# Optimization experiments

Measured on AMD Instinct MI355X. Metric: run time of the kernel, lower is better.

Reference implementation:

```python
import jax, jax.numpy as jnp
import numpy as np

BS, T, N, DIM = 16, 2048, 2048, 128

def setup_inputs() -> dict:
    key = jax.random.key(0)
    k1, k2, k3 = jax.random.split(key, 3)
    aud_feats = jax.random.normal(k1, (BS, T, DIM), dtype=jnp.float32)
    semantic_feats = jax.random.normal(k2, (BS, N, DIM), dtype=jnp.float32)
    W = jax.random.normal(k3, (1, 3 * DIM), dtype=jnp.float32) * 0.02
    b = jnp.zeros((1,), dtype=jnp.float32)
    return {"aud_feats": aud_feats, "semantic_feats": semantic_feats, "W": W, "b": b}


def reference(aud_feats, semantic_feats, W, b):
    # S[b,i,j] = Linear(cat(h_t, h_n, h_t*h_n)) decomposed into three rank-1 pieces
    dim = aud_feats.shape[-1]
    w1 = W[0, :dim]
    w2 = W[0, dim:2 * dim]
    w3 = W[0, 2 * dim:]
    S = (jnp.einsum('btd,d->bt', aud_feats, w1)[:, :, None]
         + jnp.einsum('bnd,d->bn', semantic_feats, w2)[:, None, :]
         + jnp.einsum('btd,bnd->btn', aud_feats * w3, semantic_feats)
         + b[0])  # [bs, t, n]
    at = jax.nn.softmax(S, axis=2)                     # attend over semantic tokens
    bw = jax.nn.softmax(jnp.max(S, axis=2), axis=1)    # [bs, t]
    h_con_a2 = jnp.einsum('bt,btd->bd', bw, aud_feats)[:, None, :]   # [bs,1,d], broadcasts
    h_con_w = jnp.einsum('btn,bnd->btd', at, semantic_feats)          # [bs,t,d]
    flow_matrix = jnp.concatenate(
        [aud_feats, h_con_w, aud_feats * h_con_w, aud_feats * h_con_a2], axis=2)
    return flow_matrix
```

## Files before the change

kernel.cpp:

```cpp
#include <hip/hip_runtime.h>
#include <stdint.h>

#define BSZ 16
#define TT  2048
#define NSEM 2048
#define DIM 128
#define ORS 1024
#define PSTR 68

typedef __attribute__((ext_vector_type(8))) short short8;
typedef __attribute__((ext_vector_type(4))) float floatx4;

__device__ __forceinline__ unsigned short f2bf(float f){
  unsigned u = __float_as_uint(f);
  return (unsigned short)((u + 0x7fffu + ((u >> 16) & 1u)) >> 16);
}
__device__ __forceinline__ void ld8f(const float* p, float* v){
  floatx4 a = *(const floatx4*)p;
  floatx4 b = *(const floatx4*)(p + 4);
  v[0]=a[0]; v[1]=a[1]; v[2]=a[2]; v[3]=a[3];
  v[4]=b[0]; v[5]=b[1]; v[6]=b[2]; v[7]=b[3];
}
__device__ __forceinline__ void gload_lds16(const unsigned short* g, unsigned short* l){
  __builtin_amdgcn_global_load_lds((const __attribute__((address_space(1))) void*)g,
                                   (__attribute__((address_space(3))) void*)l, 16, 0, 0);
}


__global__ __launch_bounds__(256) void prep_kernel(const float* __restrict__ sem,
                                                   const float* __restrict__ W,
                                                   float* __restrict__ colB,
                                                   unsigned short* __restrict__ outw){
  __shared__ unsigned short tile[DIM * 72];
  const int tid = threadIdx.x;
  const int b  = blockIdx.x >> 5;
  const int n0 = (blockIdx.x & 31) * 64;

  const int r = tid >> 2, cc = tid & 3, c = cc * 32;
  const float* src = sem + ((size_t)(b * NSEM + n0 + r)) * DIM + c;
  float v[32];
  ld8f(src, v); ld8f(src + 8, v + 8); ld8f(src + 16, v + 16); ld8f(src + 24, v + 24);
  alignas(16) unsigned short bf[32];
  float cpart = 0.f;
  #pragma unroll
  for (int j = 0; j < 32; ++j){
    bf[j] = f2bf(v[j]);
    cpart += v[j] * W[DIM + c + j];
  }
  {
    const int nblk = (n0 >> 4) + (r >> 4);
    const int l15r = r & 15;
    unsigned short* base = outw + ((size_t)(b * TT + nblk * 4 + cc)) * ORS + 512;
    const uint4* s4 = (const uint4*)bf;
    #pragma unroll
    for (int q = 0; q < 4; ++q)
      *(uint4*)(base + q * 128 + l15r * 8) = s4[q];
  }
  #pragma unroll
  for (int j = 0; j < 32; ++j) tile[(c + j) * 72 + r] = bf[j];
  cpart += __shfl_xor(cpart, 1);
  cpart += __shfl_xor(cpart, 2);
  if (cc == 0) colB[b * NSEM + n0 + r] = cpart;
  __syncthreads();

  {
    const int kt = tid >> 7, dc = (tid >> 4) & 7, l15 = tid & 15;
    const int d = dc * 16 + l15;
    const int ntile = n0 >> 6;
    unsigned short* base = outw + ((size_t)(b * TT + 512 + ntile * 16 + kt * 8 + dc)) * ORS + 512;
    #pragma unroll
    for (int q = 0; q < 4; ++q){
      uint4 tv = *(const uint4*)&tile[d * 72 + kt * 32 + q * 8];
      *(uint4*)(base + q * 128 + l15 * 8) = tv;
    }
  }
}

__global__ __launch_bounds__(256, 2) void flash_kernel(const float* __restrict__ aud,
                                                    const float* __restrict__ W,
                                                    const float* __restrict__ colB,
                                                    float* __restrict__ m_ws,
                                                    float* __restrict__ outf,
                                                    const unsigned short* __restrict__ outw){
  __shared__ alignas(16) unsigned short kvt[2][32][512];
  __shared__ alignas(16) unsigned short pbuf[4][16 * PSTR];

  const int tid  = threadIdx.x;
  const int wv   = tid >> 6;
  const int lane = tid & 63;
  const int quad = lane >> 4;
  const int l15  = lane & 15;
  const int b    = blockIdx.x >> 5;
  const int t0w  = (blockIdx.x & 31) * 64 + wv * 16;

  const unsigned short* stage = outw + (size_t)b * TT * ORS + 512 + lane * 8;

  #pragma unroll
  for (int jj = 0; jj < 8; ++jj){
    const int j = wv * 8 + jj;
    const int row = (j < 16) ? j : 512 + (j - 16);
    gload_lds16(stage + (size_t)row * ORS, &kvt[0][j][0]);
  }

  const float* audRow = aud + ((size_t)b * TT + t0w + l15) * DIM;
  short8 qf[4];
  float rowA_part = 0.f;
  #pragma unroll
  for (int kc = 0; kc < 4; ++kc){
    int d0 = kc * 32 + quad * 8;
    float av[8], w3v[8], w1v[8];
    ld8f(audRow + d0, av);
    ld8f(W + 2 * DIM + d0, w3v);
    ld8f(W + d0, w1v);
    alignas(16) unsigned short tmp[8];
    #pragma unroll
    for (int j = 0; j < 8; ++j){
      tmp[j] = f2bf(av[j] * w3v[j]);
      rowA_part += av[j] * w1v[j];
    }
    qf[kc] = *(const short8*)tmp;
  }
  rowA_part += __shfl_xor(rowA_part, 16);
  rowA_part += __shfl_xor(rowA_part, 32);

  float m_run = -1e30f, l_run = 0.f;
  floatx4 o[8];
  #pragma unroll
  for (int dc = 0; dc < 8; ++dc){
    #pragma unroll
    for (int r = 0; r < 4; ++r) o[dc][r] = 0.f;
  }

  const float* colBb = colB + b * NSEM;
  unsigned short* pb = &pbuf[wv][0];

  __syncthreads();

  for (int it = 0; it < 32; ++it){
    const int n0 = it * 64;
    if (it + 1 < 32){
      #pragma unroll
      for (int jj = 0; jj < 8; ++jj){
        const int j = wv * 8 + jj;
        const int row = (j < 16) ? (it + 1) * 16 + j : 512 + (it + 1) * 16 + (j - 16);
        gload_lds16(stage + (size_t)row * ORS, &kvt[(it + 1) & 1][j][0]);
      }
    }
    const unsigned short* kvb = &kvt[it & 1][0][0] + lane * 8;

    floatx4 cbv[4];
    #pragma unroll
    for (int s = 0; s < 4; ++s) cbv[s] = *(const floatx4*)(colBb + n0 + s*16 + quad*4);

    floatx4 sacc[4];
    #pragma unroll
    for (int s = 0; s < 4; ++s){ sacc[s][0]=0.f; sacc[s][1]=0.f; sacc[s][2]=0.f; sacc[s][3]=0.f; }
    #pragma unroll
    for (int s = 0; s < 4; ++s){
      #pragma unroll
      for (int kc = 0; kc < 4; ++kc){
        short8 kf = *(const short8*)(kvb + (s*4 + kc) * 512);
        sacc[s] = __builtin_amdgcn_mfma_f32_16x16x32_bf16(kf, qf[kc], sacc[s], 0, 0, 0);
      }
    }

    float v[4][4];
    #pragma unroll
    for (int s = 0; s < 4; ++s){
      #pragma unroll
      for (int r = 0; r < 4; ++r) v[s][r] = sacc[s][r] + cbv[s][r];
    }
    float mq[4];
    #pragma unroll
    for (int s = 0; s < 4; ++s)
      mq[s] = fmaxf(fmaxf(v[s][0], v[s][1]), fmaxf(v[s][2], v[s][3]));
    float mx = fmaxf(fmaxf(mq[0], mq[1]), fmaxf(mq[2], mq[3]));
    mx = fmaxf(mx, __shfl_xor(mx, 16));
    mx = fmaxf(mx, __shfl_xor(mx, 32));
    float mnew = fmaxf(m_run, mx);
    float al = __expf(m_run - mnew);
    m_run = mnew;
    float e[4][4];
    #pragma unroll
    for (int s = 0; s < 4; ++s){
      #pragma unroll
      for (int r = 0; r < 4; ++r) e[s][r] = __expf(v[s][r] - mnew);
    }
    float sq[4];
    #pragma unroll
    for (int s = 0; s < 4; ++s)
      sq[s] = (e[s][0] + e[s][1]) + (e[s][2] + e[s][3]);
    float ps = (sq[0] + sq[1]) + (sq[2] + sq[3]);
    ps += __shfl_xor(ps, 16);
    ps += __shfl_xor(ps, 32);
    l_run = l_run * al + ps;

    #pragma unroll
    for (int s = 0; s < 4; ++s){
      unsigned u0 = (unsigned)f2bf(e[s][0]) | ((unsigned)f2bf(e[s][1]) << 16);
      unsigned u1 = (unsigned)f2bf(e[s][2]) | ((unsigned)f2bf(e[s][3]) << 16);
      unsigned short* pr = pb + l15 * PSTR + s * 16 + quad * 4;
      *(unsigned*)(pr)     = u0;
      *(unsigned*)(pr + 2) = u1;
    }

    float aB[4];
    #pragma unroll
    for (int r = 0; r < 4; ++r) aB[r] = __shfl(al, quad*4 + r);
    #pragma unroll
    for (int dc = 0; dc < 8; ++dc){
      #pragma unroll
      for (int r = 0; r < 4; ++r) o[dc][r] *= aB[r];
    }

    asm volatile("s_waitcnt lgkmcnt(0)" ::: "memory");
    short8 pf0 = *(const short8*)(pb + l15 * PSTR + quad * 8);
    short8 pf1 = *(const short8*)(pb + l15 * PSTR + 32 + quad * 8);

    #pragma unroll
    for (int kt = 0; kt < 2; ++kt){
      short8 pf = kt ? pf1 : pf0;
      #pragma unroll
      for (int dc = 0; dc < 8; ++dc){
        short8 vf = *(const short8*)(kvb + (16 + kt*8 + dc) * 512);
        o[dc] = __builtin_amdgcn_mfma_f32_16x16x32_bf16(pf, vf, o[dc], 0, 0, 0);
      }
    }

    __syncthreads();
  }

  float rl = 1.0f / l_run;
  float rB[4];
  #pragma unroll
  for (int r = 0; r < 4; ++r) rB[r] = __shfl(rl, quad*4 + r);
  float* outB = outf + ((size_t)b * TT + t0w) * 512 + 128;
  #pragma unroll
  for (int dc = 0; dc < 8; ++dc){
    #pragma unroll
    for (int r = 0; r < 4; ++r)
      outB[(size_t)(quad*4 + r) * 512 + dc*16 + l15] = o[dc][r] * rB[r];
  }
  if (quad == 0)
    m_ws[(size_t)b * TT + t0w + l15] = m_run + rowA_part;
}

__global__ __launch_bounds__(256) void bw1_kernel(const float* __restrict__ m_ws,
                                                  float* __restrict__ pmax){
  __shared__ float sA[4];
  const int b = blockIdx.x >> 3, ch = blockIdx.x & 7, tid = threadIdx.x;
  float v = m_ws[(size_t)b * TT + ch * 256 + tid];
  #pragma unroll
  for (int off = 1; off < 64; off <<= 1) v = fmaxf(v, __shfl_xor(v, off));
  if ((tid & 63) == 0) sA[tid >> 6] = v;
  __syncthreads();
  if (tid == 0)
    pmax[blockIdx.x] = fmaxf(fmaxf(sA[0], sA[1]), fmaxf(sA[2], sA[3]));
}

__global__ __launch_bounds__(256) void bw2_kernel(const float* __restrict__ aud,
                                                  const float* __restrict__ m_ws,
                                                  const float* __restrict__ pmax,
                                                  float* __restrict__ gpart,
                                                  float* __restrict__ part){
  __shared__ float wbuf[256];
  __shared__ float red[16 * 128];
  __shared__ float gs4[4];
  const int b = blockIdx.x >> 3, ch = blockIdx.x & 7, tid = threadIdx.x;

  float gmax = pmax[b * 8];
  #pragma unroll
  for (int i = 1; i < 8; ++i) gmax = fmaxf(gmax, pmax[b * 8 + i]);

  float w = __expf(m_ws[(size_t)b * TT + ch * 256 + tid] - gmax);
  wbuf[tid] = w;
  float sm = w;
  #pragma unroll
  for (int off = 1; off < 64; off <<= 1) sm += __shfl_xor(sm, off);
  if ((tid & 63) == 0) gs4[tid >> 6] = sm;
  __syncthreads();
  if (tid == 0) gpart[blockIdx.x] = (gs4[0] + gs4[1]) + (gs4[2] + gs4[3]);

  const int dg = tid & 15, q = tid >> 4;
  float acc[8] = {0,0,0,0,0,0,0,0};
  const float* ab = aud + ((size_t)b * TT + ch * 256 + q * 16) * DIM + dg * 8;
  for (int i = 0; i < 16; ++i){
    float av[8];
    ld8f(ab + (size_t)i * DIM, av);
    float wt = wbuf[q * 16 + i];
    #pragma unroll
    for (int j = 0; j < 8; ++j) acc[j] += wt * av[j];
  }
  #pragma unroll
  for (int j = 0; j < 8; ++j) red[q * 128 + dg * 8 + j] = acc[j];
  __syncthreads();
  if (tid < 128){
    float s = 0.f;
    #pragma unroll
    for (int q2 = 0; q2 < 16; ++q2) s += red[q2 * 128 + tid];
    part[(size_t)blockIdx.x * 128 + tid] = s;
  }
}

__global__ __launch_bounds__(128) void bw3_kernel(const float* __restrict__ gpart,
                                                  const float* __restrict__ part,
                                                  float* __restrict__ a2_ws){
  const int b = blockIdx.x, d = threadIdx.x;
  float s = 0.f, g = 0.f;
  #pragma unroll
  for (int ch = 0; ch < 8; ++ch){
    s += part[(size_t)(b * 8 + ch) * 128 + d];
    g += gpart[b * 8 + ch];
  }
  a2_ws[b * DIM + d] = s / g;
}

__global__ __launch_bounds__(256) void epi_kernel(const float* __restrict__ aud,
                                                  const float* __restrict__ a2_ws,
                                                  float* __restrict__ out){
  int id = blockIdx.x * 256 + threadIdx.x;
  int c = id & 15;
  int t = (id >> 4) & (TT - 1);
  int b = id >> 15;
  size_t row = (size_t)b * TT + t;

  float av[8], gv[8], hv[8];
  ld8f(aud + row * DIM + c * 8, av);
  ld8f(a2_ws + b * DIM + c * 8, gv);
  ld8f(out + row * 512 + 128 + c * 8, hv);

  floatx4 o0a, o0b, o2a, o2b, o3a, o3b;
  #pragma unroll
  for (int j = 0; j < 4; ++j){
    o0a[j] = av[j];           o0b[j] = av[4+j];
    o2a[j] = av[j]*hv[j];     o2b[j] = av[4+j]*hv[4+j];
    o3a[j] = av[j]*gv[j];     o3b[j] = av[4+j]*gv[4+j];
  }
  float* ob = out + row * 512 + c * 8;
  *(floatx4*)(ob)       = o0a;  *(floatx4*)(ob + 4)   = o0b;
  *(floatx4*)(ob + 256) = o2a;  *(floatx4*)(ob + 260) = o2b;
  *(floatx4*)(ob + 384) = o3a;  *(floatx4*)(ob + 388) = o3b;
}

extern "C" void kernel_launch(void* const* d_in, const int* in_sizes, int n_in,
                              void* d_out, int out_size, void* d_ws, size_t ws_size,
                              hipStream_t stream){
  const float* aud = (const float*)d_in[0];
  const float* sem = (const float*)d_in[1];
  const float* W   = (const float*)d_in[2];
  float* out = (float*)d_out;
  unsigned short* outw = (unsigned short*)d_out;

  float* ws    = (float*)d_ws;
  float* m_ws  = ws;
  float* colB  = m_ws + (size_t)BSZ * TT;
  float* a2_ws = colB + (size_t)BSZ * NSEM;
  float* pmax  = a2_ws + BSZ * DIM;
  float* gpart = pmax + 128;
  float* part  = gpart + 128;

  prep_kernel <<<512, 256, 0, stream>>>(sem, W, colB, outw);
  flash_kernel<<<512, 256, 0, stream>>>(aud, W, colB, m_ws, out, outw);
  bw1_kernel  <<<128, 256, 0, stream>>>(m_ws, pmax);
  bw2_kernel  <<<128, 256, 0, stream>>>(aud, m_ws, pmax, gpart, part);
  bw3_kernel  <<<BSZ, 128, 0, stream>>>(gpart, part, a2_ws);
  epi_kernel  <<<(BSZ * TT * 16) / 256, 256, 0, stream>>>(aud, a2_ws, out);
}
```

Baseline: 199.1 us.

## Process two 16-row query groups per wave to reuse K/V fragments

Each wave now handles 32 query rows (two 16-row groups) instead of 16, so each K and V fragment read from LDS feeds two MFMAs. The grid halves to 256 blocks and launch bounds drop to one block per SM to allow the doubled accumulator register footprint. This cuts LDS traffic and global K/V staging per query row, at the cost of lower occupancy and fewer blocks than the 256 CUs can absorb in waves, which may hurt latency hiding.

```diff
diff --git a/kernel.cpp b/kernel.cpp
--- a/kernel.cpp
+++ b/kernel.cpp
@@ -76,22 +76,22 @@
   }
 }
 
-__global__ __launch_bounds__(256, 2) void flash_kernel(const float* __restrict__ aud,
+__global__ __launch_bounds__(256, 1) void flash_kernel(const float* __restrict__ aud,
                                                     const float* __restrict__ W,
                                                     const float* __restrict__ colB,
                                                     float* __restrict__ m_ws,
                                                     float* __restrict__ outf,
                                                     const unsigned short* __restrict__ outw){
   __shared__ alignas(16) unsigned short kvt[2][32][512];
-  __shared__ alignas(16) unsigned short pbuf[4][16 * PSTR];
+  __shared__ alignas(16) unsigned short pbuf[4][32 * PSTR];
 
   const int tid  = threadIdx.x;
   const int wv   = tid >> 6;
   const int lane = tid & 63;
   const int quad = lane >> 4;
   const int l15  = lane & 15;
-  const int b    = blockIdx.x >> 5;
-  const int t0w  = (blockIdx.x & 31) * 64 + wv * 16;
+  const int b    = blockIdx.x >> 4;
+  const int t0w  = (blockIdx.x & 15) * 128 + wv * 32;
 
   const unsigned short* stage = outw + (size_t)b * TT * ORS + 512 + lane * 8;
 
@@ -102,34 +102,40 @@
     gload_lds16(stage + (size_t)row * ORS, &kvt[0][j][0]);
   }
 
-  const float* audRow = aud + ((size_t)b * TT + t0w + l15) * DIM;
-  short8 qf[4];
-  float rowA_part = 0.f;
-  #pragma unroll
-  for (int kc = 0; kc < 4; ++kc){
-    int d0 = kc * 32 + quad * 8;
-    float av[8], w3v[8], w1v[8];
-    ld8f(audRow + d0, av);
-    ld8f(W + 2 * DIM + d0, w3v);
-    ld8f(W + d0, w1v);
-    alignas(16) unsigned short tmp[8];
-    #pragma unroll
-    for (int j = 0; j < 8; ++j){
-      tmp[j] = f2bf(av[j] * w3v[j]);
-      rowA_part += av[j] * w1v[j];
-    }
-    qf[kc] = *(const short8*)tmp;
-  }
-  rowA_part += __shfl_xor(rowA_part, 16);
-  rowA_part += __shfl_xor(rowA_part, 32);
-
-  float m_run = -1e30f, l_run = 0.f;
-  floatx4 o[8];
-  #pragma unroll
-  for (int dc = 0; dc < 8; ++dc){
-    #pragma unroll
-    for (int r = 0; r < 4; ++r) o[dc][r] = 0.f;
-  }
+  short8 qf[2][4];
+  float rowA[2];
+  #pragma unroll
+  for (int g = 0; g < 2; ++g){
+    const float* audRow = aud + ((size_t)b * TT + t0w + g * 16 + l15) * DIM;
+    float rp = 0.f;
+    #pragma unroll
+    for (int kc = 0; kc < 4; ++kc){
+      int d0 = kc * 32 + quad * 8;
+      float av[8], w3v[8], w1v[8];
+      ld8f(audRow + d0, av);
+      ld8f(W + 2 * DIM + d0, w3v);
+      ld8f(W + d0, w1v);
+      alignas(16) unsigned short tmp[8];
+      #pragma unroll
+      for (int j = 0; j < 8; ++j){
+        tmp[j] = f2bf(av[j] * w3v[j]);
+        rp += av[j] * w1v[j];
+      }
+      qf[g][kc] = *(const short8*)tmp;
+    }
+    rp += __shfl_xor(rp, 16);
+    rp += __shfl_xor(rp, 32);
+    rowA[g] = rp;
+  }
+
+  float m_run[2] = {-1e30f, -1e30f}, l_run[2] = {0.f, 0.f};
+  floatx4 o[2][8];
+  #pragma unroll
+  for (int g = 0; g < 2; ++g)
+    #pragma unroll
+    for (int dc = 0; dc < 8; ++dc)
+      #pragma unroll
+      for (int r = 0; r < 4; ++r) o[g][dc][r] = 0.f;
 
   const float* colBb = colB + b * NSEM;
   unsigned short* pb = &pbuf[wv][0];
@@ -152,97 +158,110 @@
     #pragma unroll
     for (int s = 0; s < 4; ++s) cbv[s] = *(const floatx4*)(colBb + n0 + s*16 + quad*4);
 
-    floatx4 sacc[4];
-    #pragma unroll
-    for (int s = 0; s < 4; ++s){ sacc[s][0]=0.f; sacc[s][1]=0.f; sacc[s][2]=0.f; sacc[s][3]=0.f; }
+    floatx4 sacc[2][4];
+    #pragma unroll
+    for (int g = 0; g < 2; ++g)
+      #pragma unroll
+      for (int s = 0; s < 4; ++s){ sacc[g][s][0]=0.f; sacc[g][s][1]=0.f; sacc[g][s][2]=0.f; sacc[g][s][3]=0.f; }
     #pragma unroll
     for (int s = 0; s < 4; ++s){
       #pragma unroll
       for (int kc = 0; kc < 4; ++kc){
         short8 kf = *(const short8*)(kvb + (s*4 + kc) * 512);
-        sacc[s] = __builtin_amdgcn_mfma_f32_16x16x32_bf16(kf, qf[kc], sacc[s], 0, 0, 0);
-      }
-    }
-
-    float v[4][4];
-    #pragma unroll
-    for (int s = 0; s < 4; ++s){
-      #pragma unroll
-      for (int r = 0; r < 4; ++r) v[s][r] = sacc[s][r] + cbv[s][r];
-    }
-    float mq[4];
-    #pragma unroll
-    for (int s = 0; s < 4; ++s)
-      mq[s] = fmaxf(fmaxf(v[s][0], v[s][1]), fmaxf(v[s][2], v[s][3]));
-    float mx = fmaxf(fmaxf(mq[0], mq[1]), fmaxf(mq[2], mq[3]));
-    mx = fmaxf(mx, __shfl_xor(mx, 16));
-    mx = fmaxf(mx, __shfl_xor(mx, 32));
-    float mnew = fmaxf(m_run, mx);
-    float al = __expf(m_run - mnew);
-    m_run = mnew;
-    float e[4][4];
-    #pragma unroll
-    for (int s = 0; s < 4; ++s){
-      #pragma unroll
-      for (int r = 0; r < 4; ++r) e[s][r] = __expf(v[s][r] - mnew);
-    }
-    float sq[4];
-    #pragma unroll
-    for (int s = 0; s < 4; ++s)
-      sq[s] = (e[s][0] + e[s][1]) + (e[s][2] + e[s][3]);
-    float ps = (sq[0] + sq[1]) + (sq[2] + sq[3]);
-    ps += __shfl_xor(ps, 16);
-    ps += __shfl_xor(ps, 32);
-    l_run = l_run * al + ps;
-
-    #pragma unroll
-    for (int s = 0; s < 4; ++s){
-      unsigned u0 = (unsigned)f2bf(e[s][0]) | ((unsigned)f2bf(e[s][1]) << 16);
-      unsigned u1 = (unsigned)f2bf(e[s][2]) | ((unsigned)f2bf(e[s][3]) << 16);
-      unsigned short* pr = pb + l15 * PSTR + s * 16 + quad * 4;
-      *(unsigned*)(pr)     = u0;
-      *(unsigned*)(pr + 2) = u1;
-    }
-
-    float aB[4];
-    #pragma unroll
-    for (int r = 0; r < 4; ++r) aB[r] = __shfl(al, quad*4 + r);
-    #pragma unroll
-    for (int dc = 0; dc < 8; ++dc){
-      #pragma unroll
-      for (int r = 0; r < 4; ++r) o[dc][r] *= aB[r];
+        sacc[0][s] = __builtin_amdgcn_mfma_f32_16x16x32_bf16(kf, qf[0][kc], sacc[0][s], 0, 0, 0);
+        sacc[1][s] = __builtin_amdgcn_mfma_f32_16x16x32_bf16(kf, qf[1][kc], sacc[1][s], 0, 0, 0);
+      }
+    }
+
+    float al[2];
+    #pragma unroll
+    for (int g = 0; g < 2; ++g){
+      float v[4][4];
+      #pragma unroll
+      for (int s = 0; s < 4; ++s)
+        #pragma unroll
+        for (int r = 0; r < 4; ++r) v[s][r] = sacc[g][s][r] + cbv[s][r];
+      float mq[4];
+      #pragma unroll
+      for (int s = 0; s < 4; ++s)
+        mq[s] = fmaxf(fmaxf(v[s][0], v[s][1]), fmaxf(v[s][2], v[s][3]));
+      float mx = fmaxf(fmaxf(mq[0], mq[1]), fmaxf(mq[2], mq[3]));
+      mx = fmaxf(mx, __shfl_xor(mx, 16));
+      mx = fmaxf(mx, __shfl_xor(mx, 32));
+      float mnew = fmaxf(m_run[g], mx);
+      al[g] = __expf(m_run[g] - mnew);
+      m_run[g] = mnew;
+      float e[4][4];
+      #pragma unroll
+      for (int s = 0; s < 4; ++s)
+        #pragma unroll
+        for (int r = 0; r < 4; ++r) e[s][r] = __expf(v[s][r] - mnew);
+      float sq[4];
+      #pragma unroll
+      for (int s = 0; s < 4; ++s)
+        sq[s] = (e[s][0] + e[s][1]) + (e[s][2] + e[s][3]);
+      float ps = (sq[0] + sq[1]) + (sq[2] + sq[3]);
+      ps += __shfl_xor(ps, 16);
+      ps += __shfl_xor(ps, 32);
+      l_run[g] = l_run[g] * al[g] + ps;
+
+      #pragma unroll
+      for (int s = 0; s < 4; ++s){
+        unsigned u0 = (unsigned)f2bf(e[s][0]) | ((unsigned)f2bf(e[s][1]) << 16);
+        unsigned u1 = (unsigned)f2bf(e[s][2]) | ((unsigned)f2bf(e[s][3]) << 16);
+        unsigned short* pr = pb + (g*16 + l15) * PSTR + s * 16 + quad * 4;
+        *(unsigned*)(pr)     = u0;
+        *(unsigned*)(pr + 2) = u1;
+      }
+    }
+
+    #pragma unroll
+    for (int g = 0; g < 2; ++g){
+      float aB[4];
+      #pragma unroll
+      for (int r = 0; r < 4; ++r) aB[r] = __shfl(al[g], quad*4 + r);
+      #pragma unroll
+      for (int dc = 0; dc < 8; ++dc)
+        #pragma unroll
+        for (int r = 0; r < 4; ++r) o[g][dc][r] *= aB[r];
     }
 
     asm volatile("s_waitcnt lgkmcnt(0)" ::: "memory");
-    short8 pf0 = *(const short8*)(pb + l15 * PSTR + quad * 8);
-    short8 pf1 = *(const short8*)(pb + l15 * PSTR + 32 + quad * 8);
+    short8 pf[2][2];
+    #pragma unroll
+    for (int g = 0; g < 2; ++g){
+      pf[g][0] = *(const short8*)(pb + (g*16 + l15) * PSTR + quad * 8);
+      pf[g][1] = *(const short8*)(pb + (g*16 + l15) * PSTR + 32 + quad * 8);
+    }
 
     #pragma unroll
     for (int kt = 0; kt < 2; ++kt){
-      short8 pf = kt ? pf1 : pf0;
       #pragma unroll
       for (int dc = 0; dc < 8; ++dc){
         short8 vf = *(const short8*)(kvb + (16 + kt*8 + dc) * 512);
-        o[dc] = __builtin_amdgcn_mfma_f32_16x16x32_bf16(pf, vf, o[dc], 0, 0, 0);
+        o[0][dc] = __builtin_amdgcn_mfma_f32_16x16x32_bf16(pf[0][kt], vf, o[0][dc], 0, 0, 0);
+        o[1][dc] = __builtin_amdgcn_mfma_f32_16x16x32_bf16(pf[1][kt], vf, o[1][dc], 0, 0, 0);
       }
     }
 
     __syncthreads();
   }
 
-  float rl = 1.0f / l_run;
-  float rB[4];
-  #pragma unroll
-  for (int r = 0; r < 4; ++r) rB[r] = __shfl(rl, quad*4 + r);
-  float* outB = outf + ((size_t)b * TT + t0w) * 512 + 128;
-  #pragma unroll
-  for (int dc = 0; dc < 8; ++dc){
-    #pragma unroll
-    for (int r = 0; r < 4; ++r)
-      outB[(size_t)(quad*4 + r) * 512 + dc*16 + l15] = o[dc][r] * rB[r];
-  }
-  if (quad == 0)
-    m_ws[(size_t)b * TT + t0w + l15] = m_run + rowA_part;
+  #pragma unroll
+  for (int g = 0; g < 2; ++g){
+    float rl = 1.0f / l_run[g];
+    float rB[4];
+    #pragma unroll
+    for (int r = 0; r < 4; ++r) rB[r] = __shfl(rl, quad*4 + r);
+    float* outB = outf + ((size_t)b * TT + t0w + g*16) * 512 + 128;
+    #pragma unroll
+    for (int dc = 0; dc < 8; ++dc)
+      #pragma unroll
+      for (int r = 0; r < 4; ++r)
+        outB[(size_t)(quad*4 + r) * 512 + dc*16 + l15] = o[g][dc][r] * rB[r];
+    if (quad == 0)
+      m_ws[(size_t)b * TT + t0w + g*16 + l15] = m_run[g] + rowA[g];
+  }
 }
 
 __global__ __launch_bounds__(256) void bw1_kernel(const float* __restrict__ m_ws,
@@ -360,7 +379,7 @@
   float* part  = gpart + 128;
 
   prep_kernel <<<512, 256, 0, stream>>>(sem, W, colB, outw);
-  flash_kernel<<<512, 256, 0, stream>>>(aud, W, colB, m_ws, out, outw);
+  flash_kernel<<<256, 256, 0, stream>>>(aud, W, colB, m_ws, out, outw);
   bw1_kernel  <<<128, 256, 0, stream>>>(m_ws, pmax);
   bw2_kernel  <<<128, 256, 0, stream>>>(aud, m_ws, pmax, gpart, part);
   bw3_kernel  <<<BSZ, 128, 0, stream>>>(gpart, part, a2_ws);
```

Result: slower. 213.9 us (+7.4%).

## Load V fragments directly to registers, defer softmax rescale, fuse bw3 into epilogue

Applied to the files above, without the earlier changes.

The flash kernel now stages only the K tiles through LDS and loads each wave's V fragments straight from global memory into registers. This halves the LDS footprint and removes the LDS reads in the PV loop, at the cost of extra global and L2 traffic and register pressure. It also adds a lazy online-softmax rescale: the O accumulators are rescaled only when the tile max exceeds the running max by more than 8, while the true max is tracked separately for the bw path. Finally, the bw3 reduction is folded into the epilogue kernel, which drops one launch but makes every epilogue block redo the small reduction.

```diff
diff --git a/kernel.cpp b/kernel.cpp
--- a/kernel.cpp
+++ b/kernel.cpp
@@ -82,7 +82,7 @@
                                                     float* __restrict__ m_ws,
                                                     float* __restrict__ outf,
                                                     const unsigned short* __restrict__ outw){
-  __shared__ alignas(16) unsigned short kvt[2][32][512];
+  __shared__ alignas(16) unsigned short kvt[2][16][512];
   __shared__ alignas(16) unsigned short pbuf[4][16 * PSTR];
 
   const int tid  = threadIdx.x;
@@ -96,10 +96,9 @@
   const unsigned short* stage = outw + (size_t)b * TT * ORS + 512 + lane * 8;
 
   #pragma unroll
-  for (int jj = 0; jj < 8; ++jj){
-    const int j = wv * 8 + jj;
-    const int row = (j < 16) ? j : 512 + (j - 16);
-    gload_lds16(stage + (size_t)row * ORS, &kvt[0][j][0]);
+  for (int jj = 0; jj < 4; ++jj){
+    const int j = wv * 4 + jj;
+    gload_lds16(stage + (size_t)j * ORS, &kvt[0][j][0]);
   }
 
   const float* audRow = aud + ((size_t)b * TT + t0w + l15) * DIM;
@@ -124,6 +123,7 @@
   rowA_part += __shfl_xor(rowA_part, 32);
 
   float m_run = -1e30f, l_run = 0.f;
+  float m_true = -1e30f;
   floatx4 o[8];
   #pragma unroll
   for (int dc = 0; dc < 8; ++dc){
@@ -138,14 +138,21 @@
 
   for (int it = 0; it < 32; ++it){
     const int n0 = it * 64;
+
+    const int cV = 512 + it * 16;
+    short8 vf[16];
+    #pragma unroll
+    for (int i = 0; i < 16; ++i) vf[i] = *(const short8*)(stage + (size_t)(cV + i) * ORS);
+
     if (it + 1 < 32){
       #pragma unroll
-      for (int jj = 0; jj < 8; ++jj){
-        const int j = wv * 8 + jj;
-        const int row = (j < 16) ? (it + 1) * 16 + j : 512 + (it + 1) * 16 + (j - 16);
-        gload_lds16(stage + (size_t)row * ORS, &kvt[(it + 1) & 1][j][0]);
+      for (int jj = 0; jj < 4; ++jj){
+        const int j = wv * 4 + jj;
+        gload_lds16(stage + (size_t)((it + 1) * 16 + j) * ORS, &kvt[(it + 1) & 1][j][0]);
       }
     }
+    __builtin_amdgcn_sched_barrier(0);
+
     const unsigned short* kvb = &kvt[it & 1][0][0] + lane * 8;
 
     floatx4 cbv[4];
@@ -177,14 +184,20 @@
     float mx = fmaxf(fmaxf(mq[0], mq[1]), fmaxf(mq[2], mq[3]));
     mx = fmaxf(mx, __shfl_xor(mx, 16));
     mx = fmaxf(mx, __shfl_xor(mx, 32));
-    float mnew = fmaxf(m_run, mx);
-    float al = __expf(m_run - mnew);
-    m_run = mnew;
+    m_true = fmaxf(m_true, mx);
+
+    const bool defer = (__all(mx - m_run <= 8.0f) != 0);
+    float al = 1.0f;
+    if (!defer){
+      float mnew = fmaxf(m_run, mx);
+      al = __expf(m_run - mnew);
+      m_run = mnew;
+    }
     float e[4][4];
     #pragma unroll
     for (int s = 0; s < 4; ++s){
       #pragma unroll
-      for (int r = 0; r < 4; ++r) e[s][r] = __expf(v[s][r] - mnew);
+      for (int r = 0; r < 4; ++r) e[s][r] = __expf(v[s][r] - m_run);
     }
     float sq[4];
     #pragma unroll
@@ -204,13 +217,15 @@
       *(unsigned*)(pr + 2) = u1;
     }
 
-    float aB[4];
-    #pragma unroll
-    for (int r = 0; r < 4; ++r) aB[r] = __shfl(al, quad*4 + r);
-    #pragma unroll
-    for (int dc = 0; dc < 8; ++dc){
-      #pragma unroll
-      for (int r = 0; r < 4; ++r) o[dc][r] *= aB[r];
+    if (!defer){
+      float aB[4];
+      #pragma unroll
+      for (int r = 0; r < 4; ++r) aB[r] = __shfl(al, quad*4 + r);
+      #pragma unroll
+      for (int dc = 0; dc < 8; ++dc){
+        #pragma unroll
+        for (int r = 0; r < 4; ++r) o[dc][r] *= aB[r];
+      }
     }
 
     asm volatile("s_waitcnt lgkmcnt(0)" ::: "memory");
@@ -221,10 +236,8 @@
     for (int kt = 0; kt < 2; ++kt){
       short8 pf = kt ? pf1 : pf0;
       #pragma unroll
-      for (int dc = 0; dc < 8; ++dc){
-        short8 vf = *(const short8*)(kvb + (16 + kt*8 + dc) * 512);
-        o[dc] = __builtin_amdgcn_mfma_f32_16x16x32_bf16(pf, vf, o[dc], 0, 0, 0);
-      }
+      for (int dc = 0; dc < 8; ++dc)
+        o[dc] = __builtin_amdgcn_mfma_f32_16x16x32_bf16(pf, vf[kt*8 + dc], o[dc], 0, 0, 0);
     }
 
     __syncthreads();
@@ -242,7 +255,7 @@
       outB[(size_t)(quad*4 + r) * 512 + dc*16 + l15] = o[dc][r] * rB[r];
   }
   if (quad == 0)
-    m_ws[(size_t)b * TT + t0w + l15] = m_run + rowA_part;
+    m_ws[(size_t)b * TT + t0w + l15] = m_true + rowA_part;
 }
 
 __global__ __launch_bounds__(256) void bw1_kernel(const float* __restrict__ m_ws,
@@ -302,32 +315,34 @@
   }
 }
 
-__global__ __launch_bounds__(128) void bw3_kernel(const float* __restrict__ gpart,
+__global__ __launch_bounds__(256) void epi_kernel(const float* __restrict__ aud,
+                                                  const float* __restrict__ gpart,
                                                   const float* __restrict__ part,
-                                                  float* __restrict__ a2_ws){
-  const int b = blockIdx.x, d = threadIdx.x;
-  float s = 0.f, g = 0.f;
-  #pragma unroll
-  for (int ch = 0; ch < 8; ++ch){
-    s += part[(size_t)(b * 8 + ch) * 128 + d];
-    g += gpart[b * 8 + ch];
-  }
-  a2_ws[b * DIM + d] = s / g;
-}
-
-__global__ __launch_bounds__(256) void epi_kernel(const float* __restrict__ aud,
-                                                  const float* __restrict__ a2_ws,
                                                   float* __restrict__ out){
+  __shared__ float a2s[DIM];
   int id = blockIdx.x * 256 + threadIdx.x;
   int c = id & 15;
   int t = (id >> 4) & (TT - 1);
   int b = id >> 15;
   size_t row = (size_t)b * TT + t;
 
+  if (threadIdx.x < 128){
+    const int d = threadIdx.x;
+    float s = 0.f, g = 0.f;
+    #pragma unroll
+    for (int ch = 0; ch < 8; ++ch){
+      s += part[(size_t)(b * 8 + ch) * 128 + d];
+      g += gpart[b * 8 + ch];
+    }
+    a2s[d] = s / g;
+  }
+  __syncthreads();
+
   float av[8], gv[8], hv[8];
   ld8f(aud + row * DIM + c * 8, av);
-  ld8f(a2_ws + b * DIM + c * 8, gv);
   ld8f(out + row * 512 + 128 + c * 8, hv);
+  #pragma unroll
+  for (int j = 0; j < 8; ++j) gv[j] = a2s[c * 8 + j];
 
   floatx4 o0a, o0b, o2a, o2b, o3a, o3b;
   #pragma unroll
@@ -363,6 +378,5 @@
   flash_kernel<<<512, 256, 0, stream>>>(aud, W, colB, m_ws, out, outw);
   bw1_kernel  <<<128, 256, 0, stream>>>(m_ws, pmax);
   bw2_kernel  <<<128, 256, 0, stream>>>(aud, m_ws, pmax, gpart, part);
-  bw3_kernel  <<<BSZ, 128, 0, stream>>>(gpart, part, a2_ws);
-  epi_kernel  <<<(BSZ * TT * 16) / 256, 256, 0, stream>>>(aud, a2_ws, out);
-}
+  epi_kernel  <<<(BSZ * TT * 16) / 256, 256, 0, stream>>>(aud, gpart, part, out);
+}
```

Result: no change. 197.3 us (-0.9%).
